# Optimization experiments

Hardware: AMD Instinct MI355X
Metric: run time of the kernel (lower is better)

## Reference

```python
import jax, jax.numpy as jnp
import numpy as np

S = 64        # state_dim
M = 16        # message_dim
H = 128       # hidden_unit_message_dim
HR = 128      # hidden_unit_readout_dim
NSTEPS = 10
N_NODES = 10000
N_FACTORS = 40000


def setup_inputs() -> dict:
    rng = np.random.default_rng(0)
    n, F = N_NODES, N_FACTORS
    # random undirected factor pairs (u, v) with u < v
    u = rng.integers(0, n - 1, F)
    v = rng.integers(u + 1, n)
    # var->factor directed edges: (u, i) and (v, i) for factor i
    v2f_src = np.stack([u, v], 1).ravel().astype(np.int32)          # [E]
    v2f_dst = np.repeat(np.arange(F), 2).astype(np.int32)           # [E]
    b = rng.normal(size=n).astype(np.float32)
    Juv = rng.normal(size=F).astype(np.float32)
    Jvu = rng.normal(size=F).astype(np.float32)
    feat_u = np.stack([b[u], b[v], Juv, Jvu], 1)
    feat_v = np.stack([b[v], b[u], Juv, Jvu], 1)
    feat = np.stack([feat_u, feat_v], 1).reshape(-1, 4).astype(np.float32)  # [E,4]
    p = lambda *s: (0.1 * rng.normal(size=s)).astype(np.float32)
    z = lambda *s: np.zeros(s, np.float32)
    inp = {
        'v2f_src': jnp.asarray(v2f_src), 'v2f_dst': jnp.asarray(v2f_dst),
        'f2v_src': jnp.asarray(v2f_dst), 'f2v_dst': jnp.asarray(v2f_src),
        'feat_v2f': jnp.asarray(feat), 'feat_f2v': jnp.asarray(feat),
        'n_nodes': n, 'n_factors': F,
        'Qw': jnp.asarray(p(4, M * M)), 'Qb': jnp.asarray(z(M * M)),
        'mp1_w1': jnp.asarray(p(2 * S, H)), 'mp1_b1': jnp.asarray(z(H)),
        'mp1_w2': jnp.asarray(p(H, H)), 'mp1_b2': jnp.asarray(z(H)),
        'mp1_w3': jnp.asarray(p(H, M)), 'mp1_b3': jnp.asarray(z(M)),
        'mp2_w1': jnp.asarray(p(2 * S, H)), 'mp2_b1': jnp.asarray(z(H)),
        'mp2_w2': jnp.asarray(p(H, H)), 'mp2_b2': jnp.asarray(z(H)),
        'mp2_w3': jnp.asarray(p(H, M)), 'mp2_b3': jnp.asarray(z(M)),
        'g1_wih': jnp.asarray(p(M, 3 * S)), 'g1_whh': jnp.asarray(p(S, 3 * S)),
        'g1_bih': jnp.asarray(z(3 * S)), 'g1_bhh': jnp.asarray(z(3 * S)),
        'g2_wih': jnp.asarray(p(M, 3 * S)), 'g2_whh': jnp.asarray(p(S, 3 * S)),
        'g2_bih': jnp.asarray(z(3 * S)), 'g2_bhh': jnp.asarray(z(3 * S)),
        'ro_w1': jnp.asarray(p(S, HR)), 'ro_b1': jnp.asarray(z(HR)),
        'ro_w2': jnp.asarray(p(HR, HR)), 'ro_b2': jnp.asarray(z(HR)),
        'ro_w3': jnp.asarray(p(HR, 2)), 'ro_b3': jnp.asarray(z(2)),
    }
    return inp


def _mlp(x, w1, b1, w2, b2, w3, b3):
    h = jax.nn.relu(x @ w1 + b1)
    h = jax.nn.relu(h @ w2 + b2)
    return h @ w3 + b3


def _gru(x, h, wih, whh, bih, bhh):
    # torch.nn.GRUCell gate order: r, z, n
    gi = x @ wih + bih
    gh = h @ whh + bhh
    ir, iz, inn = jnp.split(gi, 3, axis=-1)
    hr, hz, hn = jnp.split(gh, 3, axis=-1)
    r = jax.nn.sigmoid(ir + hr)
    zg = jax.nn.sigmoid(iz + hz)
    ng = jnp.tanh(inn + r * hn)
    return (1.0 - zg) * ng + zg * h


def reference(v2f_src, v2f_dst, f2v_src, f2v_dst, feat_v2f, feat_f2v,
              n_nodes, n_factors, Qw, Qb,
              mp1_w1, mp1_b1, mp1_w2, mp1_b2, mp1_w3, mp1_b3,
              mp2_w1, mp2_b1, mp2_w2, mp2_b2, mp2_w3, mp2_b3,
              g1_wih, g1_whh, g1_bih, g1_bhh,
              g2_wih, g2_whh, g2_bih, g2_bhh,
              ro_w1, ro_b1, ro_w2, ro_b2, ro_w3, ro_b3):
    var_h = jnp.zeros((n_nodes, S), feat_v2f.dtype)
    fac_h = jnp.zeros((n_factors, S), feat_v2f.dtype)
    # per-edge transform matrices are the same every step; hoist out of the loop
    q1 = (feat_v2f @ Qw + Qb).reshape(-1, M, M)  # [E, M, M]
    q2 = (feat_f2v @ Qw + Qb).reshape(-1, M, M)
    for _ in range(NSTEPS):
        # var -> factor
        x = jnp.concatenate([var_h[v2f_src], fac_h[v2f_dst]], axis=-1)  # [E, 2S]
        m = _mlp(x, mp1_w1, mp1_b1, mp1_w2, mp1_b2, mp1_w3, mp1_b3)    # [E, M]
        m = jnp.einsum('eij,ej->ei', q1, m)
        fac_msg = jax.ops.segment_sum(m, v2f_dst, num_segments=n_factors)
        fac_h = _gru(fac_msg, fac_h, g1_wih, g1_whh, g1_bih, g1_bhh)
        # factor -> var
        x = jnp.concatenate([fac_h[f2v_src], var_h[f2v_dst]], axis=-1)
        m = _mlp(x, mp2_w1, mp2_b1, mp2_w2, mp2_b2, mp2_w3, mp2_b3)
        m = jnp.einsum('eij,ej->ei', q2, m)
        var_msg = jax.ops.segment_sum(m, f2v_dst, num_segments=n_nodes)
        var_h = _gru(var_msg, var_h, g2_wih, g2_whh, g2_bih, g2_bhh)
    out = _mlp(var_h, ro_w1, ro_b1, ro_w2, ro_b2, ro_w3, ro_b3)  # [n_nodes, 2]
    return jax.nn.softmax(out, axis=1)
```

## Files before the change

### kernel.cpp

```cpp
#include <hip/hip_runtime.h>

#define NSTEPS 10

typedef __attribute__((ext_vector_type(8))) short bf16x8;
typedef __attribute__((ext_vector_type(4))) float f32x4;

__device__ __forceinline__ float sigmoidf_(float x) { return 1.0f / (1.0f + __expf(-x)); }
__device__ __forceinline__ float tanh_fast(float x) {
  const float e = __expf(2.f * x);
  return 1.f - 2.f / (e + 1.f);
}
__device__ __forceinline__ short bf16_(float x) {
  union { float f; unsigned u; } c; c.f = x;
  unsigned r = (c.u + 0x7FFFu + ((c.u >> 16) & 1u)) >> 16;
  return (short)r;
}
__device__ __forceinline__ unsigned pk2_(float a, float b) {
  union { float f; unsigned u; } ca, cb; ca.f = a; cb.f = b;
  return __builtin_amdgcn_perm(cb.u + 0x8000u, ca.u + 0x8000u, 0x07060302u);
}
__device__ __forceinline__ short pk1_(float a) {
  union { float f; unsigned u; } c; c.f = a;
  return (short)((c.u + 0x8000u) >> 16);
}
__device__ __forceinline__ float lo_(unsigned u) { union { unsigned u; float f; } c; c.u = u << 16; return c.f; }
__device__ __forceinline__ float hi_(unsigned u) { union { unsigned u; float f; } c; c.u = u & 0xffff0000u; return c.f; }

__device__ __forceinline__ f32x4 mfma_16x16x32(bf16x8 a, bf16x8 b, f32x4 c) {
  return __builtin_amdgcn_mfma_f32_16x16x32_bf16(a, b, c, 0, 0, 0);
}

#define C_W2A   0
#define C_W2B   32
#define C_W3A   64
#define C_W3B   68
#define C_ACOMB 72
#define C_W1AD  104
#define C_W1BS  120
#define C_RO1   136
#define C_RO2   152
#define C_Q     184
#define C_G1    189
#define C_G2    237
#define TOTAL_CHUNKS 285

struct PackJob { const float* src; int N; int KS; int nchunks; };
struct PackArgs {
  PackJob jb[10];
  const float* Qw; const float* Qb;
  const float* g1wih; const float* g1whh;
  const float* g2wih; const float* g2whh;
};

__device__ __forceinline__ float pack_val(const PackArgs& a, int g) {
  int c = g >> 9;
  const int r = g & 511;
  const int j = r & 7, n = (r >> 3) & 15, q = (r >> 7) & 3;
  const int kq = q * 8 + j;
  float val = 0.f;
  bool done = false;
  #pragma unroll
  for (int ji = 0; ji < 10; ++ji) {
    if (!done && c < a.jb[ji].nchunks) {
      const int ks = c % a.jb[ji].KS;
      const int nt = c / a.jb[ji].KS;
      const int k = ks * 32 + kq;
      val = a.jb[ji].src[(size_t)k * a.jb[ji].N + nt * 16 + n];
      done = true;
    }
    if (!done) c -= a.jb[ji].nchunks;
  }
  if (!done) {
    if (c < 5) {
      val = 0.f;
      if (kq < 16) val = (c < 4) ? a.Qw[c * 256 + n * 16 + kq] : a.Qb[n * 16 + kq];
    } else {
      c -= 5;
      const float* wih = (c < 48) ? a.g1wih : a.g2wih;
      const float* whh = (c < 48) ? a.g1whh : a.g2whh;
      if (c >= 48) c -= 48;
      const int nt = c / 3, ks = c % 3;
      const int k = ks * 32 + kq;
      const int ng = nt * 16 + n;
      const int gate = ng >> 6;
      const int nq = ng & 63;
      const int s = (nq & 15) * 4 + (nq >> 4);
      val = 0.f;
      if (gate == 0) {
        if (k < 16) val = wih[k * 192 + s];
        else if (k < 80) val = whh[(k - 16) * 192 + s];
      } else if (gate == 1) {
        if (k < 16) val = wih[k * 192 + 64 + s];
        else if (k < 80) val = whh[(k - 16) * 192 + 64 + s];
      } else if (gate == 2) {
        if (k < 16) val = wih[k * 192 + 128 + s];
      } else {
        if (k >= 16 && k < 80) val = whh[(k - 16) * 192 + 128 + s];
      }
    }
  }
  return val;
}

__global__ __launch_bounds__(256) void k_pack(PackArgs a, short* __restrict__ out, int total) {
  const int g = blockIdx.x * 256 + threadIdx.x;
  if (g < total) out[g] = bf16_(pack_val(a, g));
}

__device__ __forceinline__ void var_gru_tile(
    const short* wb, const float* gbih, const float* gbhh,
    const short* SA, float* gruH, short* outTile, int outStr,
    int rbase, int Nn, int lane, int wave, int m, int quad, bool writeH)
{
  f32x4 acc[16] = {};
  #pragma unroll
  for (int ks = 0; ks < 3; ++ks) {
    const bf16x8 av = *(const bf16x8*)&SA[(wave * 16 + m) * 104 + ks * 32 + quad * 8];
    #pragma unroll
    for (int nt = 0; nt < 16; ++nt)
      acc[nt] = mfma_16x16x32(av, ((const bf16x8*)(wb + C_G2 * 512))[(nt * 3 + ks) * 64 + lane], acc[nt]);
  }
  const int sb = m * 4;
  const f32x4 bir = *(const f32x4*)(gbih + sb);
  const f32x4 bhr = *(const f32x4*)(gbhh + sb);
  const f32x4 biz = *(const f32x4*)(gbih + 64 + sb);
  const f32x4 bhz = *(const f32x4*)(gbhh + 64 + sb);
  const f32x4 bi4 = *(const f32x4*)(gbih + 128 + sb);
  const f32x4 bh4 = *(const f32x4*)(gbhh + 128 + sb);
  #pragma unroll
  for (int reg = 0; reg < 4; ++reg) {
    const int lr = wave * 16 + quad * 4 + reg, rg = rbase + lr;
    uint2 pv; pv.x = 0u; pv.y = 0u;
    if (rg < Nn) {
      const f32x4 ho = *(const f32x4*)(gruH + (size_t)rg * 64 + sb);
      f32x4 hn;
      #pragma unroll
      for (int nt = 0; nt < 4; ++nt) {
        const float rr = sigmoidf_(acc[nt][reg] + bir[nt] + bhr[nt]);
        const float zz = sigmoidf_(acc[4 + nt][reg] + biz[nt] + bhz[nt]);
        const float nn = tanh_fast(acc[8 + nt][reg] + bi4[nt] + rr * (acc[12 + nt][reg] + bh4[nt]));
        hn[nt] = (1.f - zz) * nn + zz * ho[nt];
      }
      if (writeH) *(f32x4*)(gruH + (size_t)rg * 64 + sb) = hn;
      pv.x = pk2_(hn[0], hn[1]);
      pv.y = pk2_(hn[2], hn[3]);
    }
    *(uint2*)&outTile[lr * outStr + sb] = pv;
  }
}

__device__ __forceinline__ void partial_gemm_T(
    const short* chunk, const short* srcTile, int srcStr, short* Ps,
    int lane, int wave, int m, int quad)
{
  const int nt = wave & 1, mt0 = (wave >> 1) * 4;
  f32x4 acc[4] = {};
  #pragma unroll
  for (int ks = 0; ks < 2; ++ks) {
    const bf16x8 bfr = *(const bf16x8*)&srcTile[(nt * 16 + m) * srcStr + ks * 32 + quad * 8];
    #pragma unroll
    for (int j = 0; j < 4; ++j)
      acc[j] = mfma_16x16x32(((const bf16x8*)chunk)[((mt0 + j) * 2 + ks) * 64 + lane], bfr, acc[j]);
  }
  #pragma unroll
  for (int j = 0; j < 4; ++j) {
    const int col = (mt0 + j) * 16 + quad * 4;
    uint2 pv;
    pv.x = pk2_(acc[j][0], acc[j][1]);
    pv.y = pk2_(acc[j][2], acc[j][3]);
    *(uint2*)&Ps[(nt * 16 + m) * 136 + col] = pv;
  }
}

__device__ __forceinline__ void edge_tail(
    const short* wb, int cw2, int cw3,
    const float* b2, const float* b3,
    short* h1s, short* ms, const float* feats,
    int lane, int wave, int m, int quad, float* mq)
{
  {
    f32x4 acc[8] = {};
    #pragma unroll
    for (int ks = 0; ks < 4; ++ks) {
      const bf16x8 bfr = *(const bf16x8*)&h1s[(wave * 16 + m) * 136 + ks * 32 + quad * 8];
      #pragma unroll
      for (int mt = 0; mt < 8; ++mt)
        acc[mt] = mfma_16x16x32(((const bf16x8*)(wb + cw2))[(mt * 4 + ks) * 64 + lane], bfr, acc[mt]);
    }
    #pragma unroll
    for (int mt = 0; mt < 8; ++mt) {
      const int col = mt * 16 + quad * 4;
      const f32x4 bv = *(const f32x4*)(b2 + col);
      uint2 pv;
      pv.x = pk2_(fmaxf(acc[mt][0] + bv[0], 0.f), fmaxf(acc[mt][1] + bv[1], 0.f));
      pv.y = pk2_(fmaxf(acc[mt][2] + bv[2], 0.f), fmaxf(acc[mt][3] + bv[3], 0.f));
      *(uint2*)&h1s[(wave * 16 + m) * 136 + col] = pv;
    }
  }
  __syncthreads();

  f32x4 acc3 = {};
  #pragma unroll
  for (int ks = 0; ks < 4; ++ks) {
    const bf16x8 afr = *(const bf16x8*)&h1s[(wave * 16 + m) * 136 + ks * 32 + quad * 8];
    acc3 = mfma_16x16x32(afr, ((const bf16x8*)(wb + cw3))[ks * 64 + lane], acc3);
  }
  const float b3v = b3[m];
  #pragma unroll
  for (int rr = 0; rr < 4; ++rr) {
    const int row = wave * 16 + quad * 4 + rr;
    ms[row * 40 + m] = pk1_(acc3[rr] + b3v);
    ms[row * 40 + 16 + m] = 0;
  }
  __syncthreads();

  f32x4 accY[5] = {};
  {
    const bf16x8 afr = *(const bf16x8*)&ms[(wave * 16 + m) * 40 + quad * 8];
    #pragma unroll
    for (int tq = 0; tq < 5; ++tq)
      accY[tq] = mfma_16x16x32(afr, ((const bf16x8*)(wb + C_Q * 512))[tq * 64 + lane], accY[tq]);
  }
  #pragma unroll
  for (int rr = 0; rr < 4; ++rr) {
    const int row = wave * 16 + quad * 4 + rr;
    const f32x4 f = *(const f32x4*)&feats[row * 4];
    mq[rr] = accY[4][rr] + f.x * accY[0][rr] + f.y * accY[1][rr]
                         + f.z * accY[2][rr] + f.w * accY[3][rr];
  }
}

__global__ __launch_bounds__(256) void k_phaseA(
    const float* __restrict__ msgIn, float* __restrict__ msgZero,
    float* __restrict__ var_h,
    short* __restrict__ Abuf, short* __restrict__ Bbuf,
    const short* __restrict__ wb,
    const float* __restrict__ gbih, const float* __restrict__ gbhh, int N)
{
  __shared__ short SA[64 * 104];
  __shared__ short Xs[64 * 72];
  const int t = threadIdx.x, lane = t & 63, wave = t >> 6;
  const int m = lane & 15, quad = lane >> 4;
  const int rbase = blockIdx.x * 64;

  if (msgIn) {
    {
      const int r = t >> 2, q4 = t & 3, rg = rbase + r;
      #pragma unroll
      for (int i = 0; i < 6; ++i) {
        const int c = q4 * 4 + i * 16;
        f32x4 v = {0.f, 0.f, 0.f, 0.f};
        if (rg < N) {
          if (c < 16)      v = *(const f32x4*)(msgIn + (size_t)rg * 16 + c);
          else if (c < 80) v = *(const f32x4*)(var_h + (size_t)rg * 64 + (c - 16));
        }
        *(unsigned*)&SA[r * 104 + c]     = pk2_(v.x, v.y);
        *(unsigned*)&SA[r * 104 + c + 2] = pk2_(v.z, v.w);
      }
      if (rbase + r < N) {
        f32x4 z = {0.f, 0.f, 0.f, 0.f};
        *(f32x4*)(msgZero + (size_t)(rbase + r) * 16 + q4 * 4) = z;
      }
    }
    __syncthreads();
    var_gru_tile(wb, gbih, gbhh, SA, var_h, Xs, 72,
                 rbase, N, lane, wave, m, quad, true);
    __syncthreads();
  } else {
    const int r = t >> 2, q4 = t & 3, rg = rbase + r;
    #pragma unroll
    for (int i = 0; i < 4; ++i) {
      const int cc = q4 * 4 + i * 16;
      f32x4 v = {0.f, 0.f, 0.f, 0.f};
      if (rg < N) v = *(const f32x4*)(var_h + (size_t)rg * 64 + cc);
      *(unsigned*)&Xs[r * 72 + cc]     = pk2_(v.x, v.y);
      *(unsigned*)&Xs[r * 72 + cc + 2] = pk2_(v.z, v.w);
    }
    __syncthreads();
  }

  f32x4 acc[16] = {};
  #pragma unroll
  for (int ks = 0; ks < 2; ++ks) {
    const bf16x8 bfr = *(const bf16x8*)&Xs[(wave * 16 + m) * 72 + ks * 32 + quad * 8];
    #pragma unroll
    for (int mt = 0; mt < 16; ++mt)
      acc[mt] = mfma_16x16x32(((const bf16x8*)(wb + C_ACOMB * 512))[(mt * 2 + ks) * 64 + lane], bfr, acc[mt]);
  }
  const int rg = rbase + wave * 16 + m;
  if (rg < N) {
    #pragma unroll
    for (int mt = 0; mt < 16; ++mt) {
      const int col = mt * 16 + quad * 4;
      short* dst = (col < 128) ? Abuf : Bbuf;
      uint2 pv;
      pv.x = pk2_(acc[mt][0], acc[mt][1]);
      pv.y = pk2_(acc[mt][2], acc[mt][3]);
      *(uint2*)&dst[(size_t)rg * 128 + (col & 127)] = pv;
    }
  }
}

__global__ __launch_bounds__(256) void k_phaseB(
    const short* __restrict__ Abuf, const short* __restrict__ Bbuf,
    const int* __restrict__ v2f_src, const int* __restrict__ f2v_dst,
    const float* __restrict__ featA, const float* __restrict__ featB,
    const float* __restrict__ m1b1, const float* __restrict__ m1b2,
    const float* __restrict__ m1b3,
    const float* __restrict__ m2b1, const float* __restrict__ m2b2,
    const float* __restrict__ m2b3,
    const float* __restrict__ g1bih, const float* __restrict__ g1bhh,
    const short* __restrict__ wb,
    float* __restrict__ fac_h, float* __restrict__ msgV, int E, int F)
{
  __shared__ __align__(16) char smemB[38912];
  short* h1s   = (short*)(smemB);
  short* Ps    = (short*)(smemB + 17408);
  short* ms    = (short*)(smemB + 17408);
  short* AsG   = (short*)(smemB + 26112);
  short* Fs2   = (short*)(smemB + 32768);
  float* feats = (float*)(smemB + 37376);
  int*   sidx  = (int*)(smemB + 38400);
  int*   didx  = (int*)(smemB + 38656);

  const int t = threadIdx.x, lane = t & 63, wave = t >> 6;
  const int m = lane & 15, quad = lane >> 4;
  const int e0 = blockIdx.x * 64, f0 = blockIdx.x * 32;

  if (t < 64) {
    const int eg = e0 + t;
    sidx[t] = (eg < E) ? v2f_src[eg] : 0;
    didx[t] = (eg < E) ? f2v_dst[eg] : 0;
  }
  {
    const int e = t >> 2, k = t & 3, eg = e0 + e;
    feats[e * 4 + k] = (eg < E) ? featA[(size_t)eg * 4 + k] : 0.f;
  }
  {
    const int hr = t >> 3, hc = (t & 7) * 8;
    const int f = f0 + hr;
    f32x4 a0 = {0.f,0.f,0.f,0.f}, a1 = {0.f,0.f,0.f,0.f};
    if (f < F) {
      a0 = *(const f32x4*)(fac_h + (size_t)f * 64 + hc);
      a1 = *(const f32x4*)(fac_h + (size_t)f * 64 + hc + 4);
    }
    uint4 o;
    o.x = pk2_(a0.x, a0.y); o.y = pk2_(a0.z, a0.w);
    o.z = pk2_(a1.x, a1.y); o.w = pk2_(a1.z, a1.w);
    *(uint4*)&AsG[hr * 104 + 16 + hc] = o;
    if (t < 64) {
      uint4 z = make_uint4(0u, 0u, 0u, 0u);
      *(uint4*)&AsG[(t >> 1) * 104 + 80 + (t & 1) * 8] = z;
    }
  }
  __syncthreads();

  partial_gemm_T(wb + C_W1AD * 512, AsG + 16, 104, Ps, lane, wave, m, quad);
  __syncthreads();

  {
    const int r = t >> 2, q4 = t & 3;
    const bool ok = (e0 + r) < E;
    const short* pa = Abuf + (size_t)sidx[r] * 128;
    const short* pb = Ps + (r >> 1) * 136;
    #pragma unroll
    for (int i = 0; i < 4; ++i) {
      const int col = (q4 + i * 4) * 8;
      uint4 o = make_uint4(0u, 0u, 0u, 0u);
      if (ok) {
        const uint4 ua = *(const uint4*)(pa + col);
        const uint4 ub = *(const uint4*)(pb + col);
        const f32x4 ba = *(const f32x4*)(m1b1 + col);
        const f32x4 bb = *(const f32x4*)(m1b1 + col + 4);
        o.x = pk2_(fmaxf(lo_(ua.x) + lo_(ub.x) + ba.x, 0.f),
                   fmaxf(hi_(ua.x) + hi_(ub.x) + ba.y, 0.f));
        o.y = pk2_(fmaxf(lo_(ua.y) + lo_(ub.y) + ba.z, 0.f),
                   fmaxf(hi_(ua.y) + hi_(ub.y) + ba.w, 0.f));
        o.z = pk2_(fmaxf(lo_(ua.z) + lo_(ub.z) + bb.x, 0.f),
                   fmaxf(hi_(ua.z) + hi_(ub.z) + bb.y, 0.f));
        o.w = pk2_(fmaxf(lo_(ua.w) + lo_(ub.w) + bb.z, 0.f),
                   fmaxf(hi_(ua.w) + hi_(ub.w) + bb.w, 0.f));
      }
      *(uint4*)&h1s[r * 136 + col] = o;
    }
  }
  __syncthreads();

  float mq[4];
  edge_tail(wb, C_W2A * 512, C_W3A * 512, m1b2, m1b3,
            h1s, ms, feats, lane, wave, m, quad, mq);
  {
    const int fl = wave * 8 + quad * 2;
    AsG[fl * 104 + m]       = pk1_(mq[0] + mq[1]);
    AsG[(fl + 1) * 104 + m] = pk1_(mq[2] + mq[3]);
  }
  __syncthreads();

  {
    const int mtg = wave >> 1, sh = wave & 1;
    f32x4 accG[8] = {};
    #pragma unroll
    for (int ks = 0; ks < 3; ++ks) {
      const bf16x8 av = *(const bf16x8*)&AsG[(mtg * 16 + m) * 104 + ks * 32 + quad * 8];
      #pragma unroll
      for (int g = 0; g < 4; ++g)
        #pragma unroll
        for (int nt2 = 0; nt2 < 2; ++nt2) {
          const int nt = g * 4 + sh * 2 + nt2;
          accG[g * 2 + nt2] = mfma_16x16x32(
              av, ((const bf16x8*)(wb + C_G1 * 512))[(nt * 3 + ks) * 64 + lane],
              accG[g * 2 + nt2]);
        }
    }
    const int sb = m * 4 + sh * 2;
    const float br0 = g1bih[sb] + g1bhh[sb],         br1 = g1bih[sb + 1] + g1bhh[sb + 1];
    const float bz0 = g1bih[64 + sb] + g1bhh[64 + sb], bz1 = g1bih[65 + sb] + g1bhh[65 + sb];
    const float bi0 = g1bih[128 + sb], bi1 = g1bih[129 + sb];
    const float bh0 = g1bhh[128 + sb], bh1 = g1bhh[129 + sb];
    #pragma unroll
    for (int reg = 0; reg < 4; ++reg) {
      const int lr = mtg * 16 + quad * 4 + reg;
      const int f = f0 + lr;
      float hn0 = 0.f, hn1 = 0.f;
      if (f < F) {
        const float2 ho = *(const float2*)(fac_h + (size_t)f * 64 + sb);
        const float r0 = sigmoidf_(accG[0][reg] + br0);
        const float r1 = sigmoidf_(accG[1][reg] + br1);
        const float z0 = sigmoidf_(accG[2][reg] + bz0);
        const float z1 = sigmoidf_(accG[3][reg] + bz1);
        const float n0 = tanh_fast(accG[4][reg] + bi0 + r0 * (accG[6][reg] + bh0));
        const float n1 = tanh_fast(accG[5][reg] + bi1 + r1 * (accG[7][reg] + bh1));
        hn0 = (1.f - z0) * n0 + z0 * ho.x;
        hn1 = (1.f - z1) * n1 + z1 * ho.y;
        float2 hw; hw.x = hn0; hw.y = hn1;
        *(float2*)(fac_h + (size_t)f * 64 + sb) = hw;
      }
      *(unsigned*)&Fs2[lr * 72 + sb] = pk2_(hn0, hn1);
    }
  }
  {
    const int e = t >> 2, k = t & 3, eg = e0 + e;
    feats[e * 4 + k] = (eg < E) ? featB[(size_t)eg * 4 + k] : 0.f;
  }
  __syncthreads();

  partial_gemm_T(wb + C_W1BS * 512, Fs2, 72, Ps, lane, wave, m, quad);
  __syncthreads();

  {
    const int r = t >> 2, q4 = t & 3;
    const bool ok = (e0 + r) < E;
    const short* pa = Ps + (r >> 1) * 136;
    const short* pb = Bbuf + (size_t)didx[r] * 128;
    #pragma unroll
    for (int i = 0; i < 4; ++i) {
      const int col = (q4 + i * 4) * 8;
      uint4 o = make_uint4(0u, 0u, 0u, 0u);
      if (ok) {
        const uint4 ua = *(const uint4*)(pa + col);
        const uint4 ub = *(const uint4*)(pb + col);
        const f32x4 ba = *(const f32x4*)(m2b1 + col);
        const f32x4 bb = *(const f32x4*)(m2b1 + col + 4);
        o.x = pk2_(fmaxf(lo_(ua.x) + lo_(ub.x) + ba.x, 0.f),
                   fmaxf(hi_(ua.x) + hi_(ub.x) + ba.y, 0.f));
        o.y = pk2_(fmaxf(lo_(ua.y) + lo_(ub.y) + ba.z, 0.f),
                   fmaxf(hi_(ua.y) + hi_(ub.y) + ba.w, 0.f));
        o.z = pk2_(fmaxf(lo_(ua.z) + lo_(ub.z) + bb.x, 0.f),
                   fmaxf(hi_(ua.z) + hi_(ub.z) + bb.y, 0.f));
        o.w = pk2_(fmaxf(lo_(ua.w) + lo_(ub.w) + bb.z, 0.f),
                   fmaxf(hi_(ua.w) + hi_(ub.w) + bb.w, 0.f));
      }
      *(uint4*)&h1s[r * 136 + col] = o;
    }
  }
  __syncthreads();

  float mq2[4];
  edge_tail(wb, C_W2B * 512, C_W3B * 512, m2b2, m2b3,
            h1s, ms, feats, lane, wave, m, quad, mq2);
  #pragma unroll
  for (int rr = 0; rr < 4; ++rr) {
    const int erow = wave * 16 + quad * 4 + rr;
    if (e0 + erow < E)
      atomicAdd(msgV + (size_t)didx[erow] * 16 + m, mq2[rr]);
  }
}

__global__ __launch_bounds__(256) void k_readout_f(
    const float* __restrict__ gruMsg, const float* __restrict__ gruH,
    const short* __restrict__ wb,
    const float* __restrict__ gbih, const float* __restrict__ gbhh,
    const float* __restrict__ rob1, const float* __restrict__ rob2,
    const float* __restrict__ row3, const float* __restrict__ rob3,
    float* __restrict__ out, int rows)
{
  __shared__ short SA[64 * 104];
  __shared__ short SH[64 * 72];
  __shared__ short S1[64 * 136];
  __shared__ short S2[64 * 136];
  __shared__ float w3s[256];
  const int t = threadIdx.x, lane = t & 63, wave = t >> 6;
  const int m = lane & 15, quad = lane >> 4;
  const int rbase = blockIdx.x * 64;

  w3s[t] = row3[t];
  {
    const int r = t >> 2, q4 = t & 3, rg = rbase + r;
    #pragma unroll
    for (int i = 0; i < 6; ++i) {
      const int c = q4 * 4 + i * 16;
      f32x4 v = {0.f, 0.f, 0.f, 0.f};
      if (rg < rows) {
        if (c < 16)      v = *(const f32x4*)(gruMsg + (size_t)rg * 16 + c);
        else if (c < 80) v = *(const f32x4*)(gruH + (size_t)rg * 64 + (c - 16));
      }
      *(unsigned*)&SA[r * 104 + c]     = pk2_(v.x, v.y);
      *(unsigned*)&SA[r * 104 + c + 2] = pk2_(v.z, v.w);
    }
  }
  __syncthreads();
  var_gru_tile(wb, gbih, gbhh, SA, (float*)gruH, SH, 72,
               rbase, rows, lane, wave, m, quad, false);
  __syncthreads();

  {
    f32x4 acc[8] = {};
    #pragma unroll
    for (int ks = 0; ks < 2; ++ks) {
      const bf16x8 bfr = *(const bf16x8*)&SH[(wave * 16 + m) * 72 + ks * 32 + quad * 8];
      #pragma unroll
      for (int mt = 0; mt < 8; ++mt)
        acc[mt] = mfma_16x16x32(((const bf16x8*)(wb + C_RO1 * 512))[(mt * 2 + ks) * 64 + lane], bfr, acc[mt]);
    }
    #pragma unroll
    for (int mt = 0; mt < 8; ++mt) {
      const int col = mt * 16 + quad * 4;
      const f32x4 bv = *(const f32x4*)(rob1 + col);
      uint2 pv;
      pv.x = pk2_(fmaxf(acc[mt][0] + bv[0], 0.f), fmaxf(acc[mt][1] + bv[1], 0.f));
      pv.y = pk2_(fmaxf(acc[mt][2] + bv[2], 0.f), fmaxf(acc[mt][3] + bv[3], 0.f));
      *(uint2*)&S1[(wave * 16 + m) * 136 + col] = pv;
    }
  }
  __syncthreads();

  {
    f32x4 acc[8] = {};
    #pragma unroll
    for (int ks = 0; ks < 4; ++ks) {
      const bf16x8 bfr = *(const bf16x8*)&S1[(wave * 16 + m) * 136 + ks * 32 + quad * 8];
      #pragma unroll
      for (int mt = 0; mt < 8; ++mt)
        acc[mt] = mfma_16x16x32(((const bf16x8*)(wb + C_RO2 * 512))[(mt * 4 + ks) * 64 + lane], bfr, acc[mt]);
    }
    #pragma unroll
    for (int mt = 0; mt < 8; ++mt) {
      const int col = mt * 16 + quad * 4;
      const f32x4 bv = *(const f32x4*)(rob2 + col);
      uint2 pv;
      pv.x = pk2_(fmaxf(acc[mt][0] + bv[0], 0.f), fmaxf(acc[mt][1] + bv[1], 0.f));
      pv.y = pk2_(fmaxf(acc[mt][2] + bv[2], 0.f), fmaxf(acc[mt][3] + bv[3], 0.f));
      *(uint2*)&S2[(wave * 16 + m) * 136 + col] = pv;
    }
  }
  __syncthreads();

  if (t < 64) {
    const int rg = rbase + t;
    if (rg < rows) {
      float l0 = rob3[0], l1 = rob3[1];
      #pragma unroll 8
      for (int k = 0; k < 128; k += 2) {
        const unsigned u = *(const unsigned*)&S2[t * 136 + k];
        const float x0 = lo_(u), x1 = hi_(u);
        l0 = fmaf(x0, w3s[k * 2 + 0], l0);
        l1 = fmaf(x0, w3s[k * 2 + 1], l1);
        l0 = fmaf(x1, w3s[k * 2 + 2], l0);
        l1 = fmaf(x1, w3s[k * 2 + 3], l1);
      }
      const float mx = fmaxf(l0, l1);
      const float e0 = __expf(l0 - mx), e1 = __expf(l1 - mx);
      const float inv = 1.f / (e0 + e1);
      out[(size_t)rg * 2 + 0] = e0 * inv;
      out[(size_t)rg * 2 + 1] = e1 * inv;
    }
  }
}

extern "C" void kernel_launch(void* const* d_in, const int* in_sizes, int n_in,
                              void* d_out, int out_size, void* d_ws, size_t ws_size,
                              hipStream_t stream)
{
  const int*   v2f_src  = (const int*)d_in[0];
  const int*   f2v_dst  = (const int*)d_in[3];
  const float* feat_v2f = (const float*)d_in[4];
  const float* feat_f2v = (const float*)d_in[5];
  const float* Qw    = (const float*)d_in[8];
  const float* Qb    = (const float*)d_in[9];
  const float* m1w1  = (const float*)d_in[10];
  const float* m1b1  = (const float*)d_in[11];
  const float* m1w2  = (const float*)d_in[12];
  const float* m1b2  = (const float*)d_in[13];
  const float* m1w3  = (const float*)d_in[14];
  const float* m1b3  = (const float*)d_in[15];
  const float* m2w1  = (const float*)d_in[16];
  const float* m2b1  = (const float*)d_in[17];
  const float* m2w2  = (const float*)d_in[18];
  const float* m2b2  = (const float*)d_in[19];
  const float* m2w3  = (const float*)d_in[20];
  const float* m2b3  = (const float*)d_in[21];
  const float* g1wih = (const float*)d_in[22];
  const float* g1whh = (const float*)d_in[23];
  const float* g1bih = (const float*)d_in[24];
  const float* g1bhh = (const float*)d_in[25];
  const float* g2wih = (const float*)d_in[26];
  const float* g2whh = (const float*)d_in[27];
  const float* g2bih = (const float*)d_in[28];
  const float* g2bhh = (const float*)d_in[29];
  const float* row1  = (const float*)d_in[30];
  const float* rob1  = (const float*)d_in[31];
  const float* row2  = (const float*)d_in[32];
  const float* rob2  = (const float*)d_in[33];
  const float* row3  = (const float*)d_in[34];
  const float* rob3  = (const float*)d_in[35];

  const int E = in_sizes[0];
  const int N = out_size / 2;
  const int F = E / 2;

  float* wsf   = (float*)d_ws;
  float* var_h = wsf;
  float* fac_h = var_h + (size_t)N * 64;
  float* msgV  = fac_h + (size_t)F * 64;
  short* Abuf  = (short*)(msgV + (size_t)N * 16);
  short* Bbuf  = Abuf + (size_t)N * 128;
  short* wb    = Bbuf + (size_t)N * 128;

  hipMemsetAsync(var_h, 0,
                 ((size_t)N * 64 + (size_t)F * 64 + (size_t)N * 16) * sizeof(float),
                 stream);

  PackArgs pk;
  pk.jb[0] = {m1w2,            128, 4, 32};
  pk.jb[1] = {m2w2,            128, 4, 32};
  pk.jb[2] = {m1w3,             16, 4,  4};
  pk.jb[3] = {m2w3,             16, 4,  4};
  pk.jb[4] = {m1w1,            128, 2, 16};
  pk.jb[5] = {m2w1 + 64 * 128, 128, 2, 16};
  pk.jb[6] = {m1w1 + 64 * 128, 128, 2, 16};
  pk.jb[7] = {m2w1,            128, 2, 16};
  pk.jb[8] = {row1,            128, 2, 16};
  pk.jb[9] = {row2,            128, 4, 32};
  pk.Qw = Qw; pk.Qb = Qb;
  pk.g1wih = g1wih; pk.g1whh = g1whh;
  pk.g2wih = g2wih; pk.g2whh = g2whh;
  const int packTotal = TOTAL_CHUNKS * 512;
  k_pack<<<(packTotal + 255) / 256, 256, 0, stream>>>(pk, wb, packTotal);

  const int gN = (N + 63) / 64;
  const int gE = (E + 63) / 64;

  for (int step = 0; step < NSTEPS; ++step) {
    k_phaseA<<<gN, 256, 0, stream>>>(
        step ? msgV : nullptr, msgV, var_h, Abuf, Bbuf, wb, g2bih, g2bhh, N);
    k_phaseB<<<gE, 256, 0, stream>>>(
        Abuf, Bbuf, v2f_src, f2v_dst, feat_v2f, feat_f2v,
        m1b1, m1b2, m1b3, m2b1, m2b2, m2b3, g1bih, g1bhh,
        wb, fac_h, msgV, E, F);
  }

  k_readout_f<<<gN, 256, 0, stream>>>(
      msgV, var_h, wb, g2bih, g2bhh, rob1, rob2, row3, rob3, (float*)d_out, N);
}
```

Measured before the change: 693.6 us.

## Prefetch gathered rows into registers, drop shared index/feature buffers and barriers

The phase-B kernel now loads edge indices, the Abuf/Bbuf gather rows and per-edge features straight from global memory into registers, issuing the loads early so their latency overlaps the GEMM work. The shared-memory index and feature arrays are removed, Fs2 is aliased onto h1s, and shared memory shrinks to 32KB with launch bounds requesting 5 blocks. Several __syncthreads are dropped because each wave now reads only rows it wrote itself. In exchange, register pressure rises from holding prefetched rows, and removing barriers relies on the per-wave row ownership being correct.

```diff
diff --git a/kernel.cpp b/kernel.cpp
--- a/kernel.cpp
+++ b/kernel.cpp
@@ -175,7 +175,7 @@
 __device__ __forceinline__ void edge_tail(
     const short* wb, int cw2, int cw3,
     const float* b2, const float* b3,
-    short* h1s, short* ms, const float* feats,
+    short* h1s, short* ms, const float* feat_g, int e0, int E,
     int lane, int wave, int m, int quad, float* mq)
 {
   {
@@ -212,7 +212,6 @@
     ms[row * 40 + m] = pk1_(acc3[rr] + b3v);
     ms[row * 40 + 16 + m] = 0;
   }
-  __syncthreads();
 
   f32x4 accY[5] = {};
   {
@@ -224,7 +223,8 @@
   #pragma unroll
   for (int rr = 0; rr < 4; ++rr) {
     const int row = wave * 16 + quad * 4 + rr;
-    const f32x4 f = *(const f32x4*)&feats[row * 4];
+    const int er = e0 + row;
+    const f32x4 f = *(const f32x4*)(feat_g + (size_t)(er < E ? er : 0) * 4);
     mq[rr] = accY[4][rr] + f.x * accY[0][rr] + f.y * accY[1][rr]
                          + f.z * accY[2][rr] + f.w * accY[3][rr];
   }
@@ -301,7 +301,7 @@
   }
 }
 
-__global__ __launch_bounds__(256) void k_phaseB(
+__global__ __launch_bounds__(256, 5) void k_phaseB(
     const short* __restrict__ Abuf, const short* __restrict__ Bbuf,
     const int* __restrict__ v2f_src, const int* __restrict__ f2v_dst,
     const float* __restrict__ featA, const float* __restrict__ featB,
@@ -313,29 +313,35 @@
     const short* __restrict__ wb,
     float* __restrict__ fac_h, float* __restrict__ msgV, int E, int F)
 {
-  __shared__ __align__(16) char smemB[38912];
-  short* h1s   = (short*)(smemB);
-  short* Ps    = (short*)(smemB + 17408);
-  short* ms    = (short*)(smemB + 17408);
-  short* AsG   = (short*)(smemB + 26112);
-  short* Fs2   = (short*)(smemB + 32768);
-  float* feats = (float*)(smemB + 37376);
-  int*   sidx  = (int*)(smemB + 38400);
-  int*   didx  = (int*)(smemB + 38656);
+  __shared__ __align__(16) char smemB[32768];
+  short* h1s = (short*)(smemB);
+  short* Ps  = (short*)(smemB + 17408);
+  short* ms  = (short*)(smemB + 17408);
+  short* Fs2 = (short*)(smemB);
+  short* AsG = (short*)(smemB + 26112);
 
   const int t = threadIdx.x, lane = t & 63, wave = t >> 6;
   const int m = lane & 15, quad = lane >> 4;
   const int e0 = blockIdx.x * 64, f0 = blockIdx.x * 32;
-
-  if (t < 64) {
-    const int eg = e0 + t;
-    sidx[t] = (eg < E) ? v2f_src[eg] : 0;
-    didx[t] = (eg < E) ? f2v_dst[eg] : 0;
-  }
-  {
-    const int e = t >> 2, k = t & 3, eg = e0 + e;
-    feats[e * 4 + k] = (eg < E) ? featA[(size_t)eg * 4 + k] : 0.f;
-  }
+  const int r = t >> 2, q4 = t & 3;
+
+  const bool okR = (e0 + r) < E;
+  const int sidx_r = okR ? v2f_src[e0 + r] : 0;
+  const int didx_r = okR ? f2v_dst[e0 + r] : 0;
+  int aidx[4];
+  #pragma unroll
+  for (int rr = 0; rr < 4; ++rr) {
+    const int er = e0 + wave * 16 + quad * 4 + rr;
+    aidx[rr] = (er < E) ? f2v_dst[er] : 0;
+  }
+  uint4 uaP[4];
+  {
+    const short* paA = Abuf + (size_t)sidx_r * 128;
+    #pragma unroll
+    for (int i = 0; i < 4; ++i)
+      uaP[i] = *(const uint4*)(paA + (q4 + i * 4) * 8);
+  }
+
   {
     const int hr = t >> 3, hc = (t & 7) * 8;
     const int f = f0 + hr;
@@ -359,16 +365,13 @@
   __syncthreads();
 
   {
-    const int r = t >> 2, q4 = t & 3;
-    const bool ok = (e0 + r) < E;
-    const short* pa = Abuf + (size_t)sidx[r] * 128;
     const short* pb = Ps + (r >> 1) * 136;
     #pragma unroll
     for (int i = 0; i < 4; ++i) {
       const int col = (q4 + i * 4) * 8;
       uint4 o = make_uint4(0u, 0u, 0u, 0u);
-      if (ok) {
-        const uint4 ua = *(const uint4*)(pa + col);
+      if (okR) {
+        const uint4 ua = uaP[i];
         const uint4 ub = *(const uint4*)(pb + col);
         const f32x4 ba = *(const f32x4*)(m1b1 + col);
         const f32x4 bb = *(const f32x4*)(m1b1 + col + 4);
@@ -384,11 +387,17 @@
       *(uint4*)&h1s[r * 136 + col] = o;
     }
   }
-  __syncthreads();
+  uint4 ubP[4];
+  {
+    const short* paB = Bbuf + (size_t)didx_r * 128;
+    #pragma unroll
+    for (int i = 0; i < 4; ++i)
+      ubP[i] = *(const uint4*)(paB + (q4 + i * 4) * 8);
+  }
 
   float mq[4];
   edge_tail(wb, C_W2A * 512, C_W3A * 512, m1b2, m1b3,
-            h1s, ms, feats, lane, wave, m, quad, mq);
+            h1s, ms, featA, e0, E, lane, wave, m, quad, mq);
   {
     const int fl = wave * 8 + quad * 2;
     AsG[fl * 104 + m]       = pk1_(mq[0] + mq[1]);
@@ -413,7 +422,7 @@
         }
     }
     const int sb = m * 4 + sh * 2;
-    const float br0 = g1bih[sb] + g1bhh[sb],         br1 = g1bih[sb + 1] + g1bhh[sb + 1];
+    const float br0 = g1bih[sb] + g1bhh[sb],           br1 = g1bih[sb + 1] + g1bhh[sb + 1];
     const float bz0 = g1bih[64 + sb] + g1bhh[64 + sb], bz1 = g1bih[65 + sb] + g1bhh[65 + sb];
     const float bi0 = g1bih[128 + sb], bi1 = g1bih[129 + sb];
     const float bh0 = g1bhh[128 + sb], bh1 = g1bhh[129 + sb];
@@ -438,27 +447,20 @@
       *(unsigned*)&Fs2[lr * 72 + sb] = pk2_(hn0, hn1);
     }
   }
-  {
-    const int e = t >> 2, k = t & 3, eg = e0 + e;
-    feats[e * 4 + k] = (eg < E) ? featB[(size_t)eg * 4 + k] : 0.f;
-  }
   __syncthreads();
 
   partial_gemm_T(wb + C_W1BS * 512, Fs2, 72, Ps, lane, wave, m, quad);
   __syncthreads();
 
   {
-    const int r = t >> 2, q4 = t & 3;
-    const bool ok = (e0 + r) < E;
     const short* pa = Ps + (r >> 1) * 136;
-    const short* pb = Bbuf + (size_t)didx[r] * 128;
     #pragma unroll
     for (int i = 0; i < 4; ++i) {
       const int col = (q4 + i * 4) * 8;
       uint4 o = make_uint4(0u, 0u, 0u, 0u);
-      if (ok) {
+      if (okR) {
         const uint4 ua = *(const uint4*)(pa + col);
-        const uint4 ub = *(const uint4*)(pb + col);
+        const uint4 ub = ubP[i];
         const f32x4 ba = *(const f32x4*)(m2b1 + col);
         const f32x4 bb = *(const f32x4*)(m2b1 + col + 4);
         o.x = pk2_(fmaxf(lo_(ua.x) + lo_(ub.x) + ba.x, 0.f),
@@ -473,16 +475,15 @@
       *(uint4*)&h1s[r * 136 + col] = o;
     }
   }
-  __syncthreads();
 
   float mq2[4];
   edge_tail(wb, C_W2B * 512, C_W3B * 512, m2b2, m2b3,
-            h1s, ms, feats, lane, wave, m, quad, mq2);
+            h1s, ms, featB, e0, E, lane, wave, m, quad, mq2);
   #pragma unroll
   for (int rr = 0; rr < 4; ++rr) {
     const int erow = wave * 16 + quad * 4 + rr;
     if (e0 + erow < E)
-      atomicAdd(msgV + (size_t)didx[erow] * 16 + m, mq2[rr]);
+      atomicAdd(msgV + (size_t)aidx[rr] * 16 + m, mq2[rr]);
   }
 }
 
```

After: 1.038 ms. 1.5x slower.
